# Performance work log

Hardware: AMD Instinct MI355X
Metric: run time of the kernel (lower is better)

The kernel has to match this reference:

```python
import jax, jax.numpy as jnp
import numpy as np

B, S, D = 2, 2048, 2048
H, KV, HD = 16, 8, 128
N_REP = H // KV


def _rotate_half(x):
    x1, x2 = x[..., : x.shape[-1] // 2], x[..., x.shape[-1] // 2 :]
    return jnp.concatenate((-x2, x1), axis=-1)


def setup_inputs() -> dict:
    key = jax.random.key(0)
    ks = jax.random.split(key, 5)
    x = jax.random.normal(ks[0], (B, S, D), dtype=jnp.float32)
    # rotary tables (llama-style): inv_freq over half dims, duplicated
    inv_freq = 1.0 / (10000.0 ** (jnp.arange(0, HD, 2, dtype=jnp.float32) / HD))
    t = jnp.arange(S, dtype=jnp.float32)
    freqs = jnp.outer(t, inv_freq)                      # [S, HD/2]
    emb = jnp.concatenate((freqs, freqs), axis=-1)      # [S, HD]
    cos, sin = jnp.cos(emb), jnp.sin(emb)
    sc = 0.02
    Wq = jax.random.normal(ks[1], (D, H * HD), dtype=jnp.float32) * sc
    Wk = jax.random.normal(ks[2], (D, KV * HD), dtype=jnp.float32) * sc
    Wv = jax.random.normal(ks[3], (D, KV * HD), dtype=jnp.float32) * sc
    Wo = jax.random.normal(ks[4], (H * HD, D), dtype=jnp.float32) * sc
    return {"x": x, "cos": cos, "sin": sin, "Wq": Wq, "Wk": Wk, "Wv": Wv, "Wo": Wo}


def reference(x, cos, sin, Wq, Wk, Wv, Wo):
    b, s, _ = x.shape
    q = (x @ Wq).reshape(b, s, H, HD)
    k = (x @ Wk).reshape(b, s, KV, HD)
    v = (x @ Wv).reshape(b, s, KV, HD)
    # RoPE (broadcast over batch and heads; unsqueeze_dim=2 layout [b,s,h,d])
    c = cos[None, :, None, :]
    sn = sin[None, :, None, :]
    q = q * c + _rotate_half(q) * sn
    k = k * c + _rotate_half(k) * sn
    # GQA expansion (repeat_kv == interleaved repeat along head dim)
    k = jnp.repeat(k, N_REP, axis=2)
    v = jnp.repeat(v, N_REP, axis=2)
    scale = HD ** -0.5
    # causal attention (single-rank ring attention == one causal flash block)
    scores = jnp.einsum("bqhd,bkhd->bhqk", q, k) * scale
    mask = jnp.tril(jnp.ones((s, s), dtype=bool))
    scores = jnp.where(mask[None, None], scores, -jnp.inf)
    probs = jax.nn.softmax(scores, axis=-1)
    attn = jnp.einsum("bhqk,bkhd->bqhd", probs, v).reshape(b, s, H * HD)
    return attn @ Wo
```

## Files before the change

### kernel.cpp

```cpp
#include <hip/hip_runtime.h>


typedef __bf16 bf16;
typedef __bf16 bf16x4 __attribute__((ext_vector_type(4)));
typedef __bf16 bf16x8 __attribute__((ext_vector_type(8)));
typedef float floatx4 __attribute__((ext_vector_type(4)));

#define AS1(p) ((const __attribute__((address_space(1))) void*)(p))
#define AS3(p) ((__attribute__((address_space(3))) void*)(p))

__device__ __forceinline__ void load16(const void* g, void* l) {
  __builtin_amdgcn_global_load_lds(AS1(g), AS3(l), 16, 0, 0);
}

__device__ __forceinline__ void phase_barrier() {
  asm volatile("" ::: "memory");
  __builtin_amdgcn_sched_barrier(0);
  __builtin_amdgcn_s_barrier();
  __builtin_amdgcn_sched_barrier(0);
  asm volatile("" ::: "memory");
}

__global__ __launch_bounds__(256) void cvt_kernel(const float* __restrict__ in,
                                                  bf16* __restrict__ out, int n4) {
  int i = blockIdx.x * blockDim.x + threadIdx.x;
  if (i >= n4) return;
  float4 v = ((const float4*)in)[i];
  bf16x4 o = {(bf16)v.x, (bf16)v.y, (bf16)v.z, (bf16)v.w};
  ((bf16x4*)out)[i] = o;
}

__global__ __launch_bounds__(256) void wtrans_kernel(
    const float* __restrict__ Wq, const float* __restrict__ Wk,
    const float* __restrict__ Wv, const float* __restrict__ Wo,
    bf16* __restrict__ WqkvT, bf16* __restrict__ WoT) {
  __shared__ float tile[32][33];
  const int wid = blockIdx.z;
  const float* src = wid == 0 ? Wq : wid == 1 ? Wk : wid == 2 ? Wv : Wo;
  bf16* dst = wid == 0 ? WqkvT
            : wid == 1 ? WqkvT + 2048ull * 2048
            : wid == 2 ? WqkvT + 3072ull * 2048
                       : WoT;
  const int ncols = (wid == 1 || wid == 2) ? 1024 : 2048;
  const int c0 = blockIdx.x * 32, r0 = blockIdx.y * 32;
  if (c0 >= ncols) return;
  const int tx = threadIdx.x & 31, ty = threadIdx.x >> 5;
#pragma unroll
  for (int i = 0; i < 4; i++) {
    int ri = ty + i * 8;
    tile[ri][tx] = src[(long)(r0 + ri) * ncols + c0 + tx];
  }
  __syncthreads();
#pragma unroll
  for (int i = 0; i < 4; i++) {
    int ci = ty + i * 8;
    dst[(long)(c0 + ci) * 2048 + r0 + tx] = (bf16)tile[tx][ci];
  }
}

__global__ __launch_bounds__(256) void transpose_bf16(
    const bf16* __restrict__ in, bf16* __restrict__ out,
    int ldi, int ldo, long ibs, long obs) {
  __shared__ bf16 tile[32][33];
  const long ib = ibs * blockIdx.z, ob = obs * blockIdx.z;
  const int c0 = blockIdx.x * 32, r0 = blockIdx.y * 32;
  const int tx = threadIdx.x & 31, ty = threadIdx.x >> 5;
#pragma unroll
  for (int i = 0; i < 4; i++) {
    int ri = ty + i * 8;
    tile[ri][tx] = in[ib + (long)(r0 + ri) * ldi + c0 + tx];
  }
  __syncthreads();
#pragma unroll
  for (int i = 0; i < 4; i++) {
    int ci = ty + i * 8;
    out[ob + (long)(c0 + ci) * ldo + r0 + tx] = tile[tx][ci];
  }
}

template <typename CT>
__global__ __launch_bounds__(512, 2) void gemm256(
    const bf16* __restrict__ A, const bf16* __restrict__ Bt, CT* __restrict__ C,
    int M, int N, int K) {
  __shared__ __align__(1024) char smem[131072];
  const int tid = threadIdx.x;
  const int wave = tid >> 6, lane = tid & 63;
  const int quad = lane >> 4, l16 = lane & 15;
  const int wm = wave >> 2, wn = wave & 3;
  const int m0 = blockIdx.y * 256, n0 = blockIdx.x * 256;

  const int srow = (wave >> 1) * 16 + (lane >> 2);
  const int skcol = (wave & 1) * 32 + (((lane & 3) * 8) ^ ((lane & 32) ? 16 : 0));
  const int sblk = wave * 1024;

  const int qoff = (quad * 16) ^ ((l16 & 8) << 2);
  const int aoff = wm * 16384 + l16 * 64 + qoff;
  const int boff = 32768 + (wn >> 1) * 16384 + (wn & 1) * 8192 + l16 * 64 + qoff;

  auto stageA = [&](int kt, int h, int buf) {
    const bf16* g = A + (size_t)(m0 + h * 128 + srow) * K + kt * 64 + skcol;
    char* d = smem + buf * 65536 + h * 16384 + sblk;
    load16(g, d);
    load16(g + (size_t)64 * K, d + 8192);
  };
  auto stageB = [&](int kt, int h, int buf) {
    const bf16* g = Bt + (size_t)(n0 + h * 128 + srow) * K + kt * 64 + skcol;
    char* d = smem + buf * 65536 + 32768 + h * 16384 + sblk;
    load16(g, d);
    load16(g + (size_t)64 * K, d + 8192);
  };
  auto rdA = [&](int buf, int fr, int ks) {
    return *(const bf16x8*)(smem + buf * 65536 + aoff + (fr * 2 + ks) * 1024);
  };
  auto rdB = [&](int buf, int fc, int ks) {
    return *(const bf16x8*)(smem + buf * 65536 + boff + (fc * 2 + ks) * 1024);
  };

  floatx4 acc[8][4] = {};

  const int nkt = K >> 6;
  const int niter = nkt >> 1;

  stageB(0, 0, 0); stageB(0, 1, 0);
  stageA(0, 0, 0); stageA(0, 1, 0);
  stageB(1, 0, 1); stageB(1, 1, 1);
  asm volatile("s_waitcnt vmcnt(4)" ::: "memory");
  __builtin_amdgcn_s_barrier();

  for (int it = 0; it < niter; ++it) {
    const int T = 2 * it;
    const bool morek = (it < niter - 1);
#pragma unroll
    for (int c = 0; c < 2; ++c) {
      const int buf = c;
      const int tA = T + 1 + c;
      const int tB = T + 2 + c;
      const bool stA = (c == 0) || morek;

      bf16x8 a[4][2], b01[2][2], b23[2][2];

#pragma unroll
      for (int fr = 0; fr < 4; ++fr)
#pragma unroll
        for (int ks = 0; ks < 2; ++ks) a[fr][ks] = rdA(buf, fr, ks);
#pragma unroll
      for (int fc = 0; fc < 2; ++fc)
#pragma unroll
        for (int ks = 0; ks < 2; ++ks) b01[fc][ks] = rdB(buf, fc, ks);
      if (stA) stageA(tA, 0, buf ^ 1);
      phase_barrier();
      __builtin_amdgcn_s_setprio(1);
#pragma unroll
      for (int ks = 0; ks < 2; ++ks)
#pragma unroll
        for (int fr = 0; fr < 4; ++fr)
#pragma unroll
          for (int fc = 0; fc < 2; ++fc)
            acc[fr][fc] = __builtin_amdgcn_mfma_f32_16x16x32_bf16(
                a[fr][ks], b01[fc][ks], acc[fr][fc], 0, 0, 0);
      __builtin_amdgcn_s_setprio(0);
      phase_barrier();

#pragma unroll
      for (int fc = 0; fc < 2; ++fc)
#pragma unroll
        for (int ks = 0; ks < 2; ++ks) b23[fc][ks] = rdB(buf, 2 + fc, ks);
      if (stA) stageA(tA, 1, buf ^ 1);
      phase_barrier();
      __builtin_amdgcn_s_setprio(1);
#pragma unroll
      for (int ks = 0; ks < 2; ++ks)
#pragma unroll
        for (int fr = 0; fr < 4; ++fr)
#pragma unroll
          for (int fc = 0; fc < 2; ++fc)
            acc[fr][2 + fc] = __builtin_amdgcn_mfma_f32_16x16x32_bf16(
                a[fr][ks], b23[fc][ks], acc[fr][2 + fc], 0, 0, 0);
      __builtin_amdgcn_s_setprio(0);
      phase_barrier();

#pragma unroll
      for (int fr = 0; fr < 4; ++fr)
#pragma unroll
        for (int ks = 0; ks < 2; ++ks) a[fr][ks] = rdA(buf, 4 + fr, ks);
      if (morek) stageB(tB, 0, buf);
      phase_barrier();
      __builtin_amdgcn_s_setprio(1);
#pragma unroll
      for (int ks = 0; ks < 2; ++ks)
#pragma unroll
        for (int fr = 0; fr < 4; ++fr)
#pragma unroll
          for (int fc = 0; fc < 2; ++fc)
            acc[4 + fr][2 + fc] = __builtin_amdgcn_mfma_f32_16x16x32_bf16(
                a[fr][ks], b23[fc][ks], acc[4 + fr][2 + fc], 0, 0, 0);
      __builtin_amdgcn_s_setprio(0);
      phase_barrier();

      if (morek) stageB(tB, 1, buf);
      if (morek)
        asm volatile("s_waitcnt vmcnt(4)" ::: "memory");
      else
        asm volatile("s_waitcnt vmcnt(0)" ::: "memory");
      phase_barrier();
      __builtin_amdgcn_s_setprio(1);
#pragma unroll
      for (int ks = 0; ks < 2; ++ks)
#pragma unroll
        for (int fr = 0; fr < 4; ++fr)
#pragma unroll
          for (int fc = 0; fc < 2; ++fc)
            acc[4 + fr][fc] = __builtin_amdgcn_mfma_f32_16x16x32_bf16(
                a[fr][ks], b01[fc][ks], acc[4 + fr][fc], 0, 0, 0);
      __builtin_amdgcn_s_setprio(0);
      phase_barrier();
    }
  }

#pragma unroll
  for (int fr = 0; fr < 8; ++fr)
#pragma unroll
    for (int fc = 0; fc < 4; ++fc)
#pragma unroll
      for (int r = 0; r < 4; ++r) {
        int row = m0 + wm * 128 + fr * 16 + quad * 4 + r;
        int col = n0 + wn * 64 + fc * 16 + l16;
        C[(size_t)row * N + col] = (CT)acc[fr][fc][r];
      }
}

__global__ void rope_kernel(bf16* __restrict__ QKV, const float* __restrict__ cosb,
                            const float* __restrict__ sinb) {
  int idx = blockIdx.x * blockDim.x + threadIdx.x;
  if (idx >= 6291456) return;
  int nh, nhs, offc;
  if (idx < 4194304) { nh = 16; nhs = 4; offc = 0; }
  else { idx -= 4194304; nh = 8; nhs = 3; offc = 2048; }
  int d = idx & 63;
  int rest = idx >> 6;
  int hh = rest & (nh - 1);
  int bs = rest >> nhs;
  int s = bs & 2047;
  size_t base = (size_t)bs * 4096 + offc + hh * 128;
  float c0 = cosb[s * 128 + d];
  float c1 = cosb[s * 128 + d + 64];
  float s0 = sinb[s * 128 + d];
  float s1 = sinb[s * 128 + d + 64];
  float x0 = (float)QKV[base + d];
  float x1 = (float)QKV[base + d + 64];
  QKV[base + d] = (bf16)(x0 * c0 - x1 * s0);
  QKV[base + d + 64] = (bf16)(x1 * c1 + x0 * s1);
}


template <bool MASK>
__device__ __forceinline__ void attn_tile64(
    const bf16* Ksw, const bf16* Vsw, bf16* Pw, const bf16x8 (&aq)[2][4],
    const bf16x8& ones, floatx4 (&oacc)[2][8], floatx4 (&lacc)[2],
    int k0, int q0w, int l16, int quad) {
  floatx4 sacc[2][4] = {};
#pragma unroll
  for (int ks = 0; ks < 4; ks++) {
#pragma unroll
    for (int j = 0; j < 4; j++) {
      int row = j * 16 + l16;
      bf16x8 bk = *(const bf16x8*)(Ksw + row * 128 + (((ks * 4 + quad) ^ (row & 15)) * 8));
      sacc[0][j] = __builtin_amdgcn_mfma_f32_16x16x32_bf16(aq[0][ks], bk, sacc[0][j], 0, 0, 0);
      sacc[1][j] = __builtin_amdgcn_mfma_f32_16x16x32_bf16(aq[1][ks], bk, sacc[1][j], 0, 0, 0);
    }
  }
  const float C = 0.12752188659023044f;
#pragma unroll
  for (int i = 0; i < 2; i++)
#pragma unroll
    for (int r = 0; r < 4; r++) {
      int row = i * 16 + quad * 4 + r;
#pragma unroll
      for (int j = 0; j < 4; j++) {
        float p = exp2f(sacc[i][j][r] * C);
        if (MASK) {
          int key = k0 + j * 16 + l16;
          int qi = q0w + row;
          if (key > qi) p = 0.f;
        }
        int col = j * 16 + l16;
        Pw[row * 64 + (((col >> 3) ^ (row & 7)) * 8) + (col & 7)] = (bf16)p;
      }
    }
#pragma unroll
  for (int ks = 0; ks < 2; ks++) {
    bf16x8 ap0 = *(const bf16x8*)(Pw + l16 * 64 + (((ks * 4 + quad) ^ (l16 & 7)) * 8));
    bf16x8 ap1 = *(const bf16x8*)(Pw + (16 + l16) * 64 + (((ks * 4 + quad) ^ (l16 & 7)) * 8));
    lacc[0] = __builtin_amdgcn_mfma_f32_16x16x32_bf16(ap0, ones, lacc[0], 0, 0, 0);
    lacc[1] = __builtin_amdgcn_mfma_f32_16x16x32_bf16(ap1, ones, lacc[1], 0, 0, 0);
#pragma unroll
    for (int j = 0; j < 8; j++) {
      int vr = j * 16 + l16;
      bf16x8 bv = *(const bf16x8*)(Vsw + vr * 64 + (((ks * 4 + quad) ^ (vr & 7)) * 8));
      oacc[0][j] = __builtin_amdgcn_mfma_f32_16x16x32_bf16(ap0, bv, oacc[0][j], 0, 0, 0);
      oacc[1][j] = __builtin_amdgcn_mfma_f32_16x16x32_bf16(ap1, bv, oacc[1][j], 0, 0, 0);
    }
  }
}

__global__ __launch_bounds__(128) void flash_kernel(
    const bf16* __restrict__ QKV, const bf16* __restrict__ Vt, bf16* __restrict__ O,
    int* __restrict__ cnt) {
  __shared__ char smem[40960];
  __shared__ int wsh;
  bf16* Ksw = (bf16*)smem;
  bf16* Vsw = (bf16*)(smem + 16384);
  const int tid = threadIdx.x;
  const int wave = tid >> 6, lane = tid & 63, quad = lane >> 4, l16 = lane & 15;
  const int wbase = tid & ~63;
  bf16* Pw = (bf16*)(smem + 32768) + wave * 2048;
  bf16x8 ones;
#pragma unroll
  for (int e = 0; e < 8; e++) ones[e] = (bf16)1.0f;

  for (;;) {
    if (tid == 0) wsh = atomicAdd(cnt, 1);
    __syncthreads();
    const int w = wsh;
    if (w >= 1024) break;
    const int qt = 31 - (w >> 5);
    const int b = (w >> 4) & 1, h = w & 15, kvh = h >> 1;
    const int q0 = qt * 64;

#pragma unroll
    for (int u = 0; u < 8; u++) {
      int g = u * 128 + tid;
      int row = g >> 4, cc = g & 15;
      const bf16* gp = QKV + (size_t)(b * 2048 + q0 + row) * 4096 + h * 128 +
                       ((cc ^ (row & 15)) * 8);
      load16(gp, smem + (u * 128 + wbase) * 16);
    }
    __syncthreads();
    bf16x8 aq[2][4];
#pragma unroll
    for (int i = 0; i < 2; i++)
#pragma unroll
      for (int ks = 0; ks < 4; ks++) {
        int row = wave * 32 + i * 16 + l16;
        aq[i][ks] =
            *(const bf16x8*)((bf16*)smem + row * 128 + (((ks * 4 + quad) ^ (row & 15)) * 8));
      }

    floatx4 oacc[2][8] = {};
    floatx4 lacc[2] = {};
    const int q0w = q0 + wave * 32;
    const int nkt = qt + 1;

    for (int kt = 0; kt < nkt; kt++) {
      __syncthreads();
#pragma unroll
      for (int u = 0; u < 8; u++) {
        int g = u * 128 + tid;
        int row = g >> 4, cc = g & 15;
        const bf16* gp = QKV + (size_t)(b * 2048 + kt * 64 + row) * 4096 + 2048 +
                         kvh * 128 + ((cc ^ (row & 15)) * 8);
        load16(gp, (char*)Ksw + (u * 128 + wbase) * 16);
      }
#pragma unroll
      for (int u = 0; u < 8; u++) {
        int g = u * 128 + tid;
        int row = g >> 3, cc = g & 7;
        const bf16* gp = Vt + (size_t)(b * 1024 + kvh * 128 + row) * 2048 + kt * 64 +
                         ((cc ^ (row & 7)) * 8);
        load16(gp, (char*)Vsw + (u * 128 + wbase) * 16);
      }
      __syncthreads();
      if (kt == qt)
        attn_tile64<true>(Ksw, Vsw, Pw, aq, ones, oacc, lacc, kt * 64, q0w, l16, quad);
      else
        attn_tile64<false>(Ksw, Vsw, Pw, aq, ones, oacc, lacc, kt * 64, q0w, l16, quad);
    }

    float rl[2][4];
#pragma unroll
    for (int i = 0; i < 2; i++)
#pragma unroll
      for (int r = 0; r < 4; r++) rl[i][r] = 1.0f / lacc[i][r];
#pragma unroll
    for (int i = 0; i < 2; i++)
#pragma unroll
      for (int j = 0; j < 8; j++)
#pragma unroll
        for (int r = 0; r < 4; r++) {
          int s = q0w + i * 16 + quad * 4 + r;
          O[(size_t)(b * 2048 + s) * 2048 + h * 128 + j * 16 + l16] =
              (bf16)(oacc[i][j][r] * rl[i][r]);
        }
  }
}

extern "C" void kernel_launch(void* const* d_in, const int* in_sizes, int n_in,
                              void* d_out, int out_size, void* d_ws, size_t ws_size,
                              hipStream_t stream) {
  (void)in_sizes; (void)n_in; (void)out_size; (void)ws_size;
  const float* x    = (const float*)d_in[0];
  const float* cosb = (const float*)d_in[1];
  const float* sinb = (const float*)d_in[2];
  const float* Wq   = (const float*)d_in[3];
  const float* Wk   = (const float*)d_in[4];
  const float* Wv   = (const float*)d_in[5];
  const float* Wo   = (const float*)d_in[6];
  float* out = (float*)d_out;

  char* ws = (char*)d_ws;
  size_t off = 0;
  auto alloc = [&](size_t bytes) { void* p = ws + off; off += bytes; return p; };
  bf16* xb    = (bf16*)alloc(4096ull * 2048 * 2);
  bf16* WqkvT = (bf16*)alloc(4096ull * 2048 * 2);
  bf16* WoT   = (bf16*)alloc(2048ull * 2048 * 2);
  bf16* QKV   = (bf16*)alloc(4096ull * 4096 * 2);
  bf16* Vtb   = (bf16*)alloc(2048ull * 2048 * 2);
  bf16* Ab    = (bf16*)alloc(4096ull * 2048 * 2);
  int*  cnt   = (int*)alloc(256);

  cvt_kernel<<<8192, 256, 0, stream>>>(x, xb, 2097152);
  hipMemsetAsync(cnt, 0, 256, stream);

  wtrans_kernel<<<dim3(64, 64, 4), 256, 0, stream>>>(Wq, Wk, Wv, Wo, WqkvT, WoT);

  gemm256<bf16><<<dim3(16, 16), 512, 0, stream>>>(xb, WqkvT, QKV, 4096, 4096, 2048);

  rope_kernel<<<24576, 256, 0, stream>>>(QKV, cosb, sinb);

  transpose_bf16<<<dim3(32, 64, 2), 256, 0, stream>>>(
      QKV + 3072, Vtb, 4096, 2048, 2048ll * 4096, 1024ll * 2048);

  flash_kernel<<<dim3(512, 1, 1), 128, 0, stream>>>(QKV, Vtb, Ab, cnt);

  gemm256<float><<<dim3(8, 16), 512, 0, stream>>>(Ab, WoT, out, 4096, 2048, 2048);
}
```

Measured before the change: 361.8 us.

## Restructure flash attention to share K/V across GQA head pair with double buffering

The flash kernel now runs 256 threads per block, and each work item covers both query heads of one KV head for a 32-row query tile. Each loaded K/V tile is therefore reused by two heads instead of being fetched separately per head. K/V tiles are double-buffered in shared memory so the next tile's loads overlap the current tile's compute, and MFMA sections are bracketed with s_setprio. The causal work split becomes finer (32-row tiles over 64-key blocks), while shared memory grows to about 72KB, which limits occupancy.

Result: faster. 342.6 us (-5.3%).

```diff
diff --git a/kernel.cpp b/kernel.cpp
--- a/kernel.cpp
+++ b/kernel.cpp
@@ -125,7 +125,7 @@
   stageA(0, 0, 0); stageA(0, 1, 0);
   stageB(1, 0, 1); stageB(1, 1, 1);
   asm volatile("s_waitcnt vmcnt(4)" ::: "memory");
-  __builtin_amdgcn_s_barrier();
+  phase_barrier();
 
   for (int it = 0; it < niter; ++it) {
     const int T = 2 * it;
@@ -254,66 +254,61 @@
 
 
 template <bool MASK>
-__device__ __forceinline__ void attn_tile64(
-    const bf16* Ksw, const bf16* Vsw, bf16* Pw, const bf16x8 (&aq)[2][4],
-    const bf16x8& ones, floatx4 (&oacc)[2][8], floatx4 (&lacc)[2],
+__device__ __forceinline__ void attn_step32(
+    const bf16* Kc, const bf16* Vc, bf16* Pw, const bf16x8 (&aq)[4],
+    const bf16x8& ones, floatx4 (&oacc)[8], floatx4& lacc,
     int k0, int q0w, int l16, int quad) {
-  floatx4 sacc[2][4] = {};
-#pragma unroll
-  for (int ks = 0; ks < 4; ks++) {
+  floatx4 sacc[4] = {};
+  __builtin_amdgcn_s_setprio(1);
+#pragma unroll
+  for (int ks = 0; ks < 4; ks++)
 #pragma unroll
     for (int j = 0; j < 4; j++) {
       int row = j * 16 + l16;
-      bf16x8 bk = *(const bf16x8*)(Ksw + row * 128 + (((ks * 4 + quad) ^ (row & 15)) * 8));
-      sacc[0][j] = __builtin_amdgcn_mfma_f32_16x16x32_bf16(aq[0][ks], bk, sacc[0][j], 0, 0, 0);
-      sacc[1][j] = __builtin_amdgcn_mfma_f32_16x16x32_bf16(aq[1][ks], bk, sacc[1][j], 0, 0, 0);
-    }
-  }
+      bf16x8 bk = *(const bf16x8*)(Kc + row * 128 + (((ks * 4 + quad) ^ (row & 15)) * 8));
+      sacc[j] = __builtin_amdgcn_mfma_f32_16x16x32_bf16(aq[ks], bk, sacc[j], 0, 0, 0);
+    }
+  __builtin_amdgcn_s_setprio(0);
   const float C = 0.12752188659023044f;
 #pragma unroll
-  for (int i = 0; i < 2; i++)
-#pragma unroll
-    for (int r = 0; r < 4; r++) {
-      int row = i * 16 + quad * 4 + r;
-#pragma unroll
-      for (int j = 0; j < 4; j++) {
-        float p = exp2f(sacc[i][j][r] * C);
-        if (MASK) {
-          int key = k0 + j * 16 + l16;
-          int qi = q0w + row;
-          if (key > qi) p = 0.f;
-        }
-        int col = j * 16 + l16;
-        Pw[row * 64 + (((col >> 3) ^ (row & 7)) * 8) + (col & 7)] = (bf16)p;
+  for (int r = 0; r < 4; r++) {
+    int row = quad * 4 + r;
+#pragma unroll
+    for (int j = 0; j < 4; j++) {
+      float p = exp2f(sacc[j][r] * C);
+      if (MASK) {
+        int key = k0 + j * 16 + l16;
+        if (key > q0w + row) p = 0.f;
       }
-    }
+      int col = j * 16 + l16;
+      Pw[row * 64 + (((col >> 3) ^ (row & 7)) * 8) + (col & 7)] = (bf16)p;
+    }
+  }
+  __builtin_amdgcn_s_setprio(1);
 #pragma unroll
   for (int ks = 0; ks < 2; ks++) {
-    bf16x8 ap0 = *(const bf16x8*)(Pw + l16 * 64 + (((ks * 4 + quad) ^ (l16 & 7)) * 8));
-    bf16x8 ap1 = *(const bf16x8*)(Pw + (16 + l16) * 64 + (((ks * 4 + quad) ^ (l16 & 7)) * 8));
-    lacc[0] = __builtin_amdgcn_mfma_f32_16x16x32_bf16(ap0, ones, lacc[0], 0, 0, 0);
-    lacc[1] = __builtin_amdgcn_mfma_f32_16x16x32_bf16(ap1, ones, lacc[1], 0, 0, 0);
+    bf16x8 ap = *(const bf16x8*)(Pw + l16 * 64 + (((ks * 4 + quad) ^ (l16 & 7)) * 8));
+    lacc = __builtin_amdgcn_mfma_f32_16x16x32_bf16(ap, ones, lacc, 0, 0, 0);
 #pragma unroll
     for (int j = 0; j < 8; j++) {
       int vr = j * 16 + l16;
-      bf16x8 bv = *(const bf16x8*)(Vsw + vr * 64 + (((ks * 4 + quad) ^ (vr & 7)) * 8));
-      oacc[0][j] = __builtin_amdgcn_mfma_f32_16x16x32_bf16(ap0, bv, oacc[0][j], 0, 0, 0);
-      oacc[1][j] = __builtin_amdgcn_mfma_f32_16x16x32_bf16(ap1, bv, oacc[1][j], 0, 0, 0);
-    }
-  }
-}
-
-__global__ __launch_bounds__(128) void flash_kernel(
+      bf16x8 bv = *(const bf16x8*)(Vc + vr * 64 + (((ks * 4 + quad) ^ (vr & 7)) * 8));
+      oacc[j] = __builtin_amdgcn_mfma_f32_16x16x32_bf16(ap, bv, oacc[j], 0, 0, 0);
+    }
+  }
+  __builtin_amdgcn_s_setprio(0);
+}
+
+__global__ __launch_bounds__(256, 2) void flash_kernel(
     const bf16* __restrict__ QKV, const bf16* __restrict__ Vt, bf16* __restrict__ O,
     int* __restrict__ cnt) {
-  __shared__ char smem[40960];
+  __shared__ __align__(1024) char smem[73728];
   __shared__ int wsh;
-  bf16* Ksw = (bf16*)smem;
-  bf16* Vsw = (bf16*)(smem + 16384);
   const int tid = threadIdx.x;
   const int wave = tid >> 6, lane = tid & 63, quad = lane >> 4, l16 = lane & 15;
   const int wbase = tid & ~63;
-  bf16* Pw = (bf16*)(smem + 32768) + wave * 2048;
+  const int hloc = wave >> 1, rhalf = wave & 1;
+  bf16* Pw = (bf16*)(smem + 65536) + wave * 1024;
   bf16x8 ones;
 #pragma unroll
   for (int e = 0; e < 8; e++) ones[e] = (bf16)1.0f;
@@ -323,74 +318,84 @@
     __syncthreads();
     const int w = wsh;
     if (w >= 1024) break;
-    const int qt = 31 - (w >> 5);
-    const int b = (w >> 4) & 1, h = w & 15, kvh = h >> 1;
-    const int q0 = qt * 64;
-
-#pragma unroll
-    for (int u = 0; u < 8; u++) {
-      int g = u * 128 + tid;
+    const int qt = 63 - (w >> 4);
+    const int b = (w >> 3) & 1, kvh = w & 7;
+    const int h = kvh * 2 + hloc;
+    const int q0 = qt * 32;
+    const int nkt = (qt >> 1) + 1;
+
+#pragma unroll
+    for (int u = 0; u < 4; u++) {
+      int g = u * 256 + tid;
       int row = g >> 4, cc = g & 15;
-      const bf16* gp = QKV + (size_t)(b * 2048 + q0 + row) * 4096 + h * 128 +
-                       ((cc ^ (row & 15)) * 8);
-      load16(gp, smem + (u * 128 + wbase) * 16);
+      const bf16* gp = QKV + (size_t)(b * 2048 + q0 + (row & 31)) * 4096 +
+                       (kvh * 2 + (row >> 5)) * 128 + ((cc ^ (row & 15)) * 8);
+      load16(gp, smem + (u * 256 + wbase) * 16);
+    }
+    asm volatile("s_waitcnt vmcnt(0)" ::: "memory");
+    phase_barrier();
+    bf16x8 aq[4];
+    {
+      int row = hloc * 32 + rhalf * 16 + l16;
+#pragma unroll
+      for (int ks = 0; ks < 4; ks++)
+        aq[ks] = *(const bf16x8*)((const bf16*)smem + row * 128 +
+                                  (((ks * 4 + quad) ^ (row & 15)) * 8));
     }
     __syncthreads();
-    bf16x8 aq[2][4];
-#pragma unroll
-    for (int i = 0; i < 2; i++)
-#pragma unroll
-      for (int ks = 0; ks < 4; ks++) {
-        int row = wave * 32 + i * 16 + l16;
-        aq[i][ks] =
-            *(const bf16x8*)((bf16*)smem + row * 128 + (((ks * 4 + quad) ^ (row & 15)) * 8));
+
+    auto stageKV = [&](int kt, int nb) {
+      char* kd = smem + nb * 16384;
+      char* vd = smem + 32768 + nb * 16384;
+#pragma unroll
+      for (int u = 0; u < 4; u++) {
+        int g = u * 256 + tid;
+        int krow = g >> 4, kcc = g & 15;
+        const bf16* kp = QKV + (size_t)(b * 2048 + kt * 64 + krow) * 4096 + 2048 +
+                         kvh * 128 + ((kcc ^ (krow & 15)) * 8);
+        load16(kp, kd + (u * 256 + wbase) * 16);
+        int vrow = g >> 3, vcc = g & 7;
+        const bf16* vp = Vt + (size_t)(b * 1024 + kvh * 128 + vrow) * 2048 + kt * 64 +
+                         ((vcc ^ (vrow & 7)) * 8);
+        load16(vp, vd + (u * 256 + wbase) * 16);
       }
-
-    floatx4 oacc[2][8] = {};
-    floatx4 lacc[2] = {};
-    const int q0w = q0 + wave * 32;
-    const int nkt = qt + 1;
+    };
+
+    stageKV(0, 0);
+
+    floatx4 oacc[8] = {};
+    floatx4 lacc = {};
+    const int q0w = q0 + rhalf * 16;
 
     for (int kt = 0; kt < nkt; kt++) {
-      __syncthreads();
-#pragma unroll
-      for (int u = 0; u < 8; u++) {
-        int g = u * 128 + tid;
-        int row = g >> 4, cc = g & 15;
-        const bf16* gp = QKV + (size_t)(b * 2048 + kt * 64 + row) * 4096 + 2048 +
-                         kvh * 128 + ((cc ^ (row & 15)) * 8);
-        load16(gp, (char*)Ksw + (u * 128 + wbase) * 16);
+      const int cur = kt & 1;
+      if (kt + 1 < nkt) {
+        stageKV(kt + 1, cur ^ 1);
+        asm volatile("s_waitcnt vmcnt(8)" ::: "memory");
+      } else {
+        asm volatile("s_waitcnt vmcnt(0)" ::: "memory");
       }
-#pragma unroll
-      for (int u = 0; u < 8; u++) {
-        int g = u * 128 + tid;
-        int row = g >> 3, cc = g & 7;
-        const bf16* gp = Vt + (size_t)(b * 1024 + kvh * 128 + row) * 2048 + kt * 64 +
-                         ((cc ^ (row & 7)) * 8);
-        load16(gp, (char*)Vsw + (u * 128 + wbase) * 16);
+      phase_barrier();
+      const bf16* Kc = (const bf16*)(smem + cur * 16384);
+      const bf16* Vc = (const bf16*)(smem + 32768 + cur * 16384);
+      if (kt == nkt - 1)
+        attn_step32<true>(Kc, Vc, Pw, aq, ones, oacc, lacc, kt * 64, q0w, l16, quad);
+      else
+        attn_step32<false>(Kc, Vc, Pw, aq, ones, oacc, lacc, kt * 64, q0w, l16, quad);
+      phase_barrier();
+    }
+
+    float rl[4];
+#pragma unroll
+    for (int r = 0; r < 4; r++) rl[r] = 1.0f / lacc[r];
+#pragma unroll
+    for (int j = 0; j < 8; j++)
+#pragma unroll
+      for (int r = 0; r < 4; r++) {
+        int s = q0w + quad * 4 + r;
+        O[(size_t)(b * 2048 + s) * 2048 + h * 128 + j * 16 + l16] =
+            (bf16)(oacc[j][r] * rl[r]);
       }
-      __syncthreads();
-      if (kt == qt)
-        attn_tile64<true>(Ksw, Vsw, Pw, aq, ones, oacc, lacc, kt * 64, q0w, l16, quad);
-      else
-        attn_tile64<false>(Ksw, Vsw, Pw, aq, ones, oacc, lacc, kt * 64, q0w, l16, quad);
-    }
-
-    float rl[2][4];
-#pragma unroll
-    for (int i = 0; i < 2; i++)
-#pragma unroll
-      for (int r = 0; r < 4; r++) rl[i][r] = 1.0f / lacc[i][r];
-#pragma unroll
-    for (int i = 0; i < 2; i++)
-#pragma unroll
-      for (int j = 0; j < 8; j++)
-#pragma unroll
-        for (int r = 0; r < 4; r++) {
-          int s = q0w + i * 16 + quad * 4 + r;
-          O[(size_t)(b * 2048 + s) * 2048 + h * 128 + j * 16 + l16] =
-              (bf16)(oacc[i][j][r] * rl[i][r]);
-        }
   }
 }
 
@@ -430,7 +435,7 @@
   transpose_bf16<<<dim3(32, 64, 2), 256, 0, stream>>>(
       QKV + 3072, Vtb, 4096, 2048, 2048ll * 4096, 1024ll * 2048);
 
-  flash_kernel<<<dim3(512, 1, 1), 128, 0, stream>>>(QKV, Vtb, Ab, cnt);
+  flash_kernel<<<dim3(512, 1, 1), 256, 0, stream>>>(QKV, Vtb, Ab, cnt);
 
   gemm256<float><<<dim3(8, 16), 512, 0, stream>>>(Ab, WoT, out, 4096, 2048, 2048);
 }
```

## Share K/V tiles across GQA head pair, double-buffer KV, static scheduling

Applied to the files above, without the earlier changes.

The flash kernel now handles both query heads that share a KV head in one 256-thread block, so each K/V tile is loaded once for two heads. K/V loads are double-buffered so the next tile is fetched while the current one is computed. The atomic work-queue is replaced by a static grid mapping that pairs long and short causal q-tiles, and wave priority is raised around the MFMA sections. This cuts global K/V traffic and exposed load latency, at the cost of doubled shared memory (80KB), which limits occupancy, and a fixed scheduling order that may leave load imbalance.

Result: faster. 352.4 us (-2.6%).

```diff
diff --git a/kernel.cpp b/kernel.cpp
--- a/kernel.cpp
+++ b/kernel.cpp
@@ -125,7 +125,7 @@
   stageA(0, 0, 0); stageA(0, 1, 0);
   stageB(1, 0, 1); stageB(1, 1, 1);
   asm volatile("s_waitcnt vmcnt(4)" ::: "memory");
-  __builtin_amdgcn_s_barrier();
+  phase_barrier();
 
   for (int it = 0; it < niter; ++it) {
     const int T = 2 * it;
@@ -259,6 +259,7 @@
     const bf16x8& ones, floatx4 (&oacc)[2][8], floatx4 (&lacc)[2],
     int k0, int q0w, int l16, int quad) {
   floatx4 sacc[2][4] = {};
+  __builtin_amdgcn_s_setprio(1);
 #pragma unroll
   for (int ks = 0; ks < 4; ks++) {
 #pragma unroll
@@ -269,6 +270,7 @@
       sacc[1][j] = __builtin_amdgcn_mfma_f32_16x16x32_bf16(aq[1][ks], bk, sacc[1][j], 0, 0, 0);
     }
   }
+  __builtin_amdgcn_s_setprio(0);
   const float C = 0.12752188659023044f;
 #pragma unroll
   for (int i = 0; i < 2; i++)
@@ -287,6 +289,7 @@
         Pw[row * 64 + (((col >> 3) ^ (row & 7)) * 8) + (col & 7)] = (bf16)p;
       }
     }
+  __builtin_amdgcn_s_setprio(1);
 #pragma unroll
   for (int ks = 0; ks < 2; ks++) {
     bf16x8 ap0 = *(const bf16x8*)(Pw + l16 * 64 + (((ks * 4 + quad) ^ (l16 & 7)) * 8));
@@ -301,97 +304,106 @@
       oacc[1][j] = __builtin_amdgcn_mfma_f32_16x16x32_bf16(ap1, bv, oacc[1][j], 0, 0, 0);
     }
   }
-}
-
-__global__ __launch_bounds__(128) void flash_kernel(
-    const bf16* __restrict__ QKV, const bf16* __restrict__ Vt, bf16* __restrict__ O,
-    int* __restrict__ cnt) {
-  __shared__ char smem[40960];
-  __shared__ int wsh;
-  bf16* Ksw = (bf16*)smem;
-  bf16* Vsw = (bf16*)(smem + 16384);
+  __builtin_amdgcn_s_setprio(0);
+}
+
+__global__ __launch_bounds__(256, 2) void flash_kernel(
+    const bf16* __restrict__ QKV, const bf16* __restrict__ Vt, bf16* __restrict__ O) {
+  __shared__ __align__(1024) char smem[81920];
   const int tid = threadIdx.x;
   const int wave = tid >> 6, lane = tid & 63, quad = lane >> 4, l16 = lane & 15;
   const int wbase = tid & ~63;
-  bf16* Pw = (bf16*)(smem + 32768) + wave * 2048;
+  const int hloc = wave >> 1, rhalf = wave & 1;
+  bf16* Pw = (bf16*)(smem + 65536) + wave * 2048;
   bf16x8 ones;
 #pragma unroll
   for (int e = 0; e < 8; e++) ones[e] = (bf16)1.0f;
 
-  for (;;) {
-    if (tid == 0) wsh = atomicAdd(cnt, 1);
-    __syncthreads();
-    const int w = wsh;
-    if (w >= 1024) break;
-    const int qt = 31 - (w >> 5);
-    const int b = (w >> 4) & 1, h = w & 15, kvh = h >> 1;
-    const int q0 = qt * 64;
-
-#pragma unroll
-    for (int u = 0; u < 8; u++) {
-      int g = u * 128 + tid;
-      int row = g >> 4, cc = g & 15;
-      const bf16* gp = QKV + (size_t)(b * 2048 + q0 + row) * 4096 + h * 128 +
-                       ((cc ^ (row & 15)) * 8);
-      load16(gp, smem + (u * 128 + wbase) * 16);
-    }
-    __syncthreads();
-    bf16x8 aq[2][4];
-#pragma unroll
-    for (int i = 0; i < 2; i++)
-#pragma unroll
-      for (int ks = 0; ks < 4; ks++) {
-        int row = wave * 32 + i * 16 + l16;
-        aq[i][ks] =
-            *(const bf16x8*)((bf16*)smem + row * 128 + (((ks * 4 + quad) ^ (row & 15)) * 8));
+  const int w = blockIdx.x;
+  const int g = w >> 4;
+  const int qt = (g < 16) ? (31 - g) : (g - 16);
+  const int b = (w >> 3) & 1, kvh = w & 7;
+  const int h = kvh * 2 + hloc;
+  const int q0 = qt * 64;
+  const int nkt = qt + 1;
+
+#pragma unroll
+  for (int u = 0; u < 8; u++) {
+    int gg = u * 256 + tid;
+    int row = gg >> 4, cc = gg & 15;
+    const bf16* gp = QKV + (size_t)(b * 2048 + q0 + (row & 63)) * 4096 +
+                     (kvh * 2 + (row >> 6)) * 128 + ((cc ^ (row & 15)) * 8);
+    load16(gp, smem + (u * 256 + wbase) * 16);
+  }
+  asm volatile("s_waitcnt vmcnt(0)" ::: "memory");
+  phase_barrier();
+  bf16x8 aq[2][4];
+#pragma unroll
+  for (int i = 0; i < 2; i++)
+#pragma unroll
+    for (int ks = 0; ks < 4; ks++) {
+      int qr = hloc * 64 + rhalf * 32 + i * 16 + l16;
+      aq[i][ks] = *(const bf16x8*)((const bf16*)smem + qr * 128 +
+                                   (((ks * 4 + quad) ^ (qr & 15)) * 8));
+    }
+  __syncthreads();
+
+  auto stageKV = [&](int kt, int nb) {
+    char* kd = smem + nb * 16384;
+    char* vd = smem + 32768 + nb * 16384;
+#pragma unroll
+    for (int u = 0; u < 4; u++) {
+      int gg = u * 256 + tid;
+      int krow = gg >> 4, kcc = gg & 15;
+      const bf16* kp = QKV + (size_t)(b * 2048 + kt * 64 + krow) * 4096 + 2048 +
+                       kvh * 128 + ((kcc ^ (krow & 15)) * 8);
+      load16(kp, kd + (u * 256 + wbase) * 16);
+      int vrow = gg >> 3, vcc = gg & 7;
+      const bf16* vp = Vt + (size_t)(b * 1024 + kvh * 128 + vrow) * 2048 + kt * 64 +
+                       ((vcc ^ (vrow & 7)) * 8);
+      load16(vp, vd + (u * 256 + wbase) * 16);
+    }
+  };
+
+  stageKV(0, 0);
+
+  floatx4 oacc[2][8] = {};
+  floatx4 lacc[2] = {};
+  const int q0w = q0 + rhalf * 32;
+
+  for (int kt = 0; kt < nkt; kt++) {
+    const int cur = kt & 1;
+    if (kt + 1 < nkt) {
+      stageKV(kt + 1, cur ^ 1);
+      asm volatile("s_waitcnt vmcnt(8)" ::: "memory");
+    } else {
+      asm volatile("s_waitcnt vmcnt(0)" ::: "memory");
+    }
+    phase_barrier();
+    const bf16* Kc = (const bf16*)(smem + cur * 16384);
+    const bf16* Vc = (const bf16*)(smem + 32768 + cur * 16384);
+    if (kt == nkt - 1)
+      attn_tile64<true>(Kc, Vc, Pw, aq, ones, oacc, lacc, kt * 64, q0w, l16, quad);
+    else
+      attn_tile64<false>(Kc, Vc, Pw, aq, ones, oacc, lacc, kt * 64, q0w, l16, quad);
+    phase_barrier();
+  }
+
+  float rl[2][4];
+#pragma unroll
+  for (int i = 0; i < 2; i++)
+#pragma unroll
+    for (int r = 0; r < 4; r++) rl[i][r] = 1.0f / lacc[i][r];
+#pragma unroll
+  for (int i = 0; i < 2; i++)
+#pragma unroll
+    for (int j = 0; j < 8; j++)
+#pragma unroll
+      for (int r = 0; r < 4; r++) {
+        int s = q0w + i * 16 + quad * 4 + r;
+        O[(size_t)(b * 2048 + s) * 2048 + h * 128 + j * 16 + l16] =
+            (bf16)(oacc[i][j][r] * rl[i][r]);
       }
-
-    floatx4 oacc[2][8] = {};
-    floatx4 lacc[2] = {};
-    const int q0w = q0 + wave * 32;
-    const int nkt = qt + 1;
-
-    for (int kt = 0; kt < nkt; kt++) {
-      __syncthreads();
-#pragma unroll
-      for (int u = 0; u < 8; u++) {
-        int g = u * 128 + tid;
-        int row = g >> 4, cc = g & 15;
-        const bf16* gp = QKV + (size_t)(b * 2048 + kt * 64 + row) * 4096 + 2048 +
-                         kvh * 128 + ((cc ^ (row & 15)) * 8);
-        load16(gp, (char*)Ksw + (u * 128 + wbase) * 16);
-      }
-#pragma unroll
-      for (int u = 0; u < 8; u++) {
-        int g = u * 128 + tid;
-        int row = g >> 3, cc = g & 7;
-        const bf16* gp = Vt + (size_t)(b * 1024 + kvh * 128 + row) * 2048 + kt * 64 +
-                         ((cc ^ (row & 7)) * 8);
-        load16(gp, (char*)Vsw + (u * 128 + wbase) * 16);
-      }
-      __syncthreads();
-      if (kt == qt)
-        attn_tile64<true>(Ksw, Vsw, Pw, aq, ones, oacc, lacc, kt * 64, q0w, l16, quad);
-      else
-        attn_tile64<false>(Ksw, Vsw, Pw, aq, ones, oacc, lacc, kt * 64, q0w, l16, quad);
-    }
-
-    float rl[2][4];
-#pragma unroll
-    for (int i = 0; i < 2; i++)
-#pragma unroll
-      for (int r = 0; r < 4; r++) rl[i][r] = 1.0f / lacc[i][r];
-#pragma unroll
-    for (int i = 0; i < 2; i++)
-#pragma unroll
-      for (int j = 0; j < 8; j++)
-#pragma unroll
-        for (int r = 0; r < 4; r++) {
-          int s = q0w + i * 16 + quad * 4 + r;
-          O[(size_t)(b * 2048 + s) * 2048 + h * 128 + j * 16 + l16] =
-              (bf16)(oacc[i][j][r] * rl[i][r]);
-        }
-  }
 }
 
 extern "C" void kernel_launch(void* const* d_in, const int* in_sizes, int n_in,
@@ -416,10 +428,8 @@
   bf16* QKV   = (bf16*)alloc(4096ull * 4096 * 2);
   bf16* Vtb   = (bf16*)alloc(2048ull * 2048 * 2);
   bf16* Ab    = (bf16*)alloc(4096ull * 2048 * 2);
-  int*  cnt   = (int*)alloc(256);
 
   cvt_kernel<<<8192, 256, 0, stream>>>(x, xb, 2097152);
-  hipMemsetAsync(cnt, 0, 256, stream);
 
   wtrans_kernel<<<dim3(64, 64, 4), 256, 0, stream>>>(Wq, Wk, Wv, Wo, WqkvT, WoT);
 
@@ -430,7 +440,7 @@
   transpose_bf16<<<dim3(32, 64, 2), 256, 0, stream>>>(
       QKV + 3072, Vtb, 4096, 2048, 2048ll * 4096, 1024ll * 2048);
 
-  flash_kernel<<<dim3(512, 1, 1), 128, 0, stream>>>(QKV, Vtb, Ab, cnt);
+  flash_kernel<<<dim3(512, 1, 1), 256, 0, stream>>>(QKV, Vtb, Ab);
 
   gemm256<float><<<dim3(8, 16), 512, 0, stream>>>(Ab, WoT, out, 4096, 2048, 2048);
 }
```
